# Performance work log

Measured on AMD Instinct MI355X. Metric: run time of the kernel, lower is better.

## Reference

```python
import jax, jax.numpy as jnp
import numpy as np

N, E, M, A, D = 100000, 3200000, 4096, 32, 16
G, V1, V2, O1 = 10, 20, 10, 20


def _lin(key, fin, fout, scale=0.1):
    kw, kb = jax.random.split(key)
    W = jax.random.normal(kw, (fin, fout), jnp.float32) * scale
    b = jax.random.normal(kb, (fout,), jnp.float32) * scale
    return W, b


def setup_inputs():
    key = jax.random.key(0)
    ks = jax.random.split(key, 32)
    inp = {}
    inp["x1"] = jax.random.normal(ks[0], (N, 15), jnp.float32)
    inp["x2"] = jax.random.normal(ks[1], (4,), jnp.float32)
    inp["edges"] = jax.random.randint(ks[2], (2, E), 0, N)
    inp["attack_src"] = jax.random.randint(ks[3], (M, A), 0, N)
    inp["attack_dst"] = jax.random.randint(ks[4], (M, A), 0, N)
    inp["attack_armies"] = jax.random.uniform(ks[5], (M, A), jnp.float32, 1.0, 20.0)
    inp["deploy_target"] = jax.random.randint(ks[6], (M, D), 0, N)
    inp["deploy_armies"] = jax.random.uniform(ks[7], (M, D), jnp.float32, 1.0, 10.0)
    inp["init_W"], inp["init_b"] = _lin(ks[8], 15, G)
    for i, fin in zip((1, 2, 3), (G + 15, 2 * G + 15, 3 * G + 15)):
        k1, k2, k3, k4 = jax.random.split(ks[8 + i], 4)
        inp[f"g{i}_Wl"] = jax.random.normal(k1, (fin, G), jnp.float32) * 0.1
        inp[f"g{i}_Wr"] = jax.random.normal(k2, (fin, G), jnp.float32) * 0.1
        inp[f"g{i}_att"] = jax.random.normal(k3, (G,), jnp.float32) * 0.1
        inp[f"g{i}_b"] = jax.random.normal(k4, (G,), jnp.float32) * 0.1
    inp["vt_W"], inp["vt_b"] = _lin(ks[12], 15 + G + 4, V1)
    inp["va_W"], inp["va_b"] = _lin(ks[13], V1, 1)
    inp["vv_W"], inp["vv_b"] = _lin(ks[14], V1, V2)
    inp["vl_W"], inp["vl_b"] = _lin(ks[15], V2, 1)
    inp["at_W"], inp["at_b"] = _lin(ks[16], 48, O1)
    inp["dt_W"], inp["dt_b"] = _lin(ks[17], 23, O1)
    inp["oa_W"], inp["oa_b"] = _lin(ks[18], O1, 1)
    inp["ov_W"], inp["ov_b"] = _lin(ks[19], O1, 1)
    return inp


def _gatv2(x, src, dst, Wl, Wr, att, bias, n):
    # GATv2 (PyG defaults: heads=1, negative_slope=0.2); dropout omitted (eval mode)
    xl = x @ Wl  # source-side transform  [N, G]
    xr = x @ Wr  # target-side transform  [N, G]
    e = jax.nn.leaky_relu(xl[src] + xr[dst], 0.2) @ att  # [Etot]
    emax = jax.ops.segment_max(e, dst, num_segments=n)
    ex = jnp.exp(e - emax[dst])
    denom = jax.ops.segment_sum(ex, dst, num_segments=n)
    alpha = ex / denom[dst]  # edge softmax per target node
    return jax.ops.segment_sum(alpha[:, None] * xl[src], dst, num_segments=n) + bias


def _forward(x1, x2, edges, attack_src, attack_dst, attack_armies,
             deploy_target, deploy_armies, p):
    n = x1.shape[0]
    loop = jnp.arange(n)
    src = jnp.concatenate([edges[0], loop])  # add_self_loops (PyG default)
    dst = jnp.concatenate([edges[1], loop])
    x_ = jax.nn.relu(x1 @ p["init_W"] + p["init_b"])  # Dropout = identity in eval
    xa = jax.nn.relu(_gatv2(jnp.concatenate([x_, x1], 1), src, dst,
                            p["g1_Wl"], p["g1_Wr"], p["g1_att"], p["g1_b"], n))
    xb = jax.nn.relu(_gatv2(jnp.concatenate([xa, x_, x1], 1), src, dst,
                            p["g2_Wl"], p["g2_Wr"], p["g2_att"], p["g2_b"], n))
    xc = jax.nn.relu(_gatv2(jnp.concatenate([xb, xa, x_, x1], 1), src, dst,
                            p["g3_Wl"], p["g3_Wr"], p["g3_att"], p["g3_b"], n))
    # per-move order features, batched over all moves at once: [M,A,*] / [M,D,*]
    x1d = x1[attack_dst]  # [M, A, 15]
    extra = 0.6 * attack_armies - 0.7 * (x1d[..., 3] + x1d[..., 4])
    att_feat = jnp.concatenate([xc[attack_src], xc[attack_dst],
                                x1[attack_src][..., 3:], x1d[..., 1:],
                                attack_armies[..., None], extra[..., None]], -1)  # [M,A,48]
    dep_feat = jnp.concatenate([xc[deploy_target], x1[deploy_target][..., 3:],
                                deploy_armies[..., None]], -1)  # [M,D,23]
    orders = jax.nn.relu(jnp.concatenate(
        [att_feat @ p["at_W"] + p["at_b"], dep_feat @ p["dt_W"] + p["dt_b"]], 1))  # [M,A+D,O1]
    oattn = jax.nn.softmax(orders @ p["oa_W"] + p["oa_b"], axis=1)  # softmax over orders
    pm = jnp.sum(oattn * (orders @ p["ov_W"] + p["ov_b"]), axis=(1, 2))  # [M]
    # value head: attention-pool over nodes
    vfeat = jnp.concatenate([xc, x1, jnp.tile(x2, (n, 1))], 1)  # [N, 29]
    v = jax.nn.relu(vfeat @ p["vt_W"] + p["vt_b"])
    vattn = jax.nn.softmax(v @ p["va_W"] + p["va_b"], axis=0)
    vagg = jax.nn.relu(jnp.sum(vattn * (v @ p["vv_W"] + p["vv_b"]), axis=0))
    V = jnp.tanh(vagg @ p["vl_W"] + p["vl_b"]).reshape(())
    return V, jax.nn.log_softmax(pm)


def reference(x1, x2, edges, attack_src, attack_dst, attack_armies,
              deploy_target, deploy_armies,
              init_W, init_b,
              g1_Wl, g1_Wr, g1_att, g1_b,
              g2_Wl, g2_Wr, g2_att, g2_b,
              g3_Wl, g3_Wr, g3_att, g3_b,
              vt_W, vt_b, va_W, va_b, vv_W, vv_b, vl_W, vl_b,
              at_W, at_b, dt_W, dt_b, oa_W, oa_b, ov_W, ov_b):
    p = dict(init_W=init_W, init_b=init_b,
             g1_Wl=g1_Wl, g1_Wr=g1_Wr, g1_att=g1_att, g1_b=g1_b,
             g2_Wl=g2_Wl, g2_Wr=g2_Wr, g2_att=g2_att, g2_b=g2_b,
             g3_Wl=g3_Wl, g3_Wr=g3_Wr, g3_att=g3_att, g3_b=g3_b,
             vt_W=vt_W, vt_b=vt_b, va_W=va_W, va_b=va_b, vv_W=vv_W, vv_b=vv_b,
             vl_W=vl_W, vl_b=vl_b, at_W=at_W, at_b=at_b, dt_W=dt_W, dt_b=dt_b,
             oa_W=oa_W, oa_b=oa_b, ov_W=ov_W, ov_b=ov_b)
    return _forward(x1, x2, edges, attack_src, attack_dst, attack_armies,
                    deploy_target, deploy_armies, p)
```

## Files before the change

kernel.cpp:

```cpp
#include <hip/hip_runtime.h>
#include <math.h>


#define PAD 12
#define LP 8
#define MAXB 784
#define CHK 8192

__device__ __forceinline__ float lrelu02(float v) { return v > 0.f ? v : 0.2f * v; }

__device__ __forceinline__ unsigned pk_bf16(float a, float b)
{
    unsigned ua = __float_as_uint(a), ub = __float_as_uint(b);
    ua += 0x7fffu + ((ua >> 16) & 1u);
    ub += 0x7fffu + ((ub >> 16) & 1u);
    return (ua >> 16) | (ub & 0xffff0000u);
}
__device__ __forceinline__ float bf_lo(unsigned u) { return __uint_as_float(u << 16); }
__device__ __forceinline__ float bf_hi(unsigned u) { return __uint_as_float(u & 0xffff0000u); }

template <int NS>
__device__ __forceinline__ void transform_body(
    int n, const float* __restrict__ s0, const float* __restrict__ s1,
    const float* __restrict__ s2, const float* __restrict__ x1,
    const float* __restrict__ Wl, const float* __restrict__ Wr,
    unsigned* __restrict__ XLb, float* __restrict__ XR)
{
    float al[10], ar[10];
#pragma unroll
    for (int g = 0; g < 10; ++g) { al[g] = 0.f; ar[g] = 0.f; }
    int o = 0;
#define TB_BLOCK(SP)                                                        \
    {                                                                       \
        const float4* pr = (const float4*)((SP) + n * PAD);                 \
        float4 v0 = pr[0], v1 = pr[1], v2 = pr[2];                          \
        float fv[10] = {v0.x, v0.y, v0.z, v0.w, v1.x, v1.y, v1.z, v1.w,     \
                        v2.x, v2.y};                                        \
        _Pragma("unroll") for (int k = 0; k < 10; ++k)                      \
        {                                                                   \
            _Pragma("unroll") for (int g = 0; g < 10; ++g)                  \
            {                                                               \
                al[g] += fv[k] * Wl[(o + k) * 10 + g];                      \
                ar[g] += fv[k] * Wr[(o + k) * 10 + g];                      \
            }                                                               \
        }                                                                   \
        o += 10;                                                            \
    }
    if constexpr (NS >= 1) TB_BLOCK(s0)
    if constexpr (NS >= 2) TB_BLOCK(s1)
    if constexpr (NS >= 3) TB_BLOCK(s2)
#undef TB_BLOCK
#pragma unroll
    for (int k = 0; k < 15; ++k) {
        float fv = x1[n * 15 + k];
#pragma unroll
        for (int g = 0; g < 10; ++g) {
            al[g] += fv * Wl[(o + k) * 10 + g];
            ar[g] += fv * Wr[(o + k) * 10 + g];
        }
    }
    uint4 q0;
    q0.x = pk_bf16(al[0], al[1]);
    q0.y = pk_bf16(al[2], al[3]);
    q0.z = pk_bf16(al[4], al[5]);
    q0.w = pk_bf16(al[6], al[7]);
    uint4 q1;
    q1.x = pk_bf16(al[8], al[9]);
    q1.y = 0; q1.z = 0; q1.w = 0;
    uint4* pb = (uint4*)(XLb + (size_t)n * LP);
    pb[0] = q0;
    pb[1] = q1;
    float4* po = (float4*)(XR + n * PAD);
    po[0] = make_float4(ar[0], ar[1], ar[2], ar[3]);
    po[1] = make_float4(ar[4], ar[5], ar[6], ar[7]);
    po[2] = make_float4(ar[8], ar[9], 0.f, 0.f);
}

__global__ __launch_bounds__(256) void k_a1_init(
    const int* __restrict__ edst, int E, unsigned short* __restrict__ pos,
    int* __restrict__ cntg, int PA,
    const float* __restrict__ x1, const float* __restrict__ W,
    const float* __restrict__ b, float* __restrict__ xo, int N, int NBK)
{
    if ((int)blockIdx.x < PA) {
        __shared__ int h[MAXB];
        for (int j = threadIdx.x; j < NBK; j += 256) h[j] = 0;
        __syncthreads();
        int base = blockIdx.x * CHK;
        for (int k = 0; k < CHK / 256; ++k) {
            int i = base + k * 256 + threadIdx.x;
            if (i < E) {
                int bkt = edst[i] >> 7;
                int p = atomicAdd(&h[bkt], 1);
                pos[i] = (unsigned short)p;
            }
        }
        __syncthreads();
        for (int j = threadIdx.x; j < NBK; j += 256)
            cntg[(size_t)j * PA + blockIdx.x] = h[j];
    } else {
        int n = ((int)blockIdx.x - PA) * 256 + (int)threadIdx.x;
        if (n >= N) return;
        float acc[10];
#pragma unroll
        for (int g = 0; g < 10; ++g) acc[g] = b[g];
#pragma unroll
        for (int k = 0; k < 15; ++k) {
            float fv = x1[n * 15 + k];
#pragma unroll
            for (int g = 0; g < 10; ++g) acc[g] += fv * W[k * 10 + g];
        }
        float4* po = (float4*)(xo + n * PAD);
        po[0] = make_float4(fmaxf(acc[0], 0.f), fmaxf(acc[1], 0.f),
                            fmaxf(acc[2], 0.f), fmaxf(acc[3], 0.f));
        po[1] = make_float4(fmaxf(acc[4], 0.f), fmaxf(acc[5], 0.f),
                            fmaxf(acc[6], 0.f), fmaxf(acc[7], 0.f));
        po[2] = make_float4(fmaxf(acc[8], 0.f), fmaxf(acc[9], 0.f), 0.f, 0.f);
    }
}

__global__ __launch_bounds__(1024) void k_scanA(
    const int* __restrict__ cntg, int* __restrict__ bases,
    int* __restrict__ bsumA, int TOT)
{
    __shared__ int wsum[16];
    int t = threadIdx.x;
    int i = blockIdx.x * 1024 + t;
    int lane = t & 63, w = t >> 6;
    int x = (i < TOT) ? cntg[i] : 0;
    int incl = x;
#pragma unroll
    for (int off = 1; off < 64; off <<= 1) {
        int u = __shfl_up(incl, off);
        if (lane >= off) incl += u;
    }
    if (lane == 63) wsum[w] = incl;
    __syncthreads();
    int woff = 0;
    for (int k = 0; k < w; ++k) woff += wsum[k];
    incl += woff;
    if (i < TOT) bases[i] = incl - x;
    if (t == 1023) bsumA[blockIdx.x] = incl;
}

__global__ __launch_bounds__(512) void k_scanB(
    const int* __restrict__ bsumA, int* __restrict__ boffA, int NBLKA,
    float* __restrict__ vsums, int* __restrict__ rowptr, int N, int Etot)
{
    __shared__ int wsum[8];
    int t = threadIdx.x;
    int lane = t & 63, w = t >> 6;
    int x = (t < NBLKA) ? bsumA[t] : 0;
    int incl = x;
#pragma unroll
    for (int off = 1; off < 64; off <<= 1) {
        int u = __shfl_up(incl, off);
        if (lane >= off) incl += u;
    }
    if (lane == 63) wsum[w] = incl;
    __syncthreads();
    int woff = 0;
    for (int k = 0; k < w; ++k) woff += wsum[k];
    incl += woff;
    if (t < NBLKA) boffA[t] = incl - x;
    if (t < 16) vsums[t] = 0.f;
    if (t == 0) rowptr[N] = Etot;
}

__global__ __launch_bounds__(1024) void k_scanC(
    int* __restrict__ bases, const int* __restrict__ boffA, int TOT)
{
    int i = blockIdx.x * 1024 + threadIdx.x;
    if (i < TOT) bases[i] += boffA[blockIdx.x];
}

__global__ __launch_bounds__(256) void k_a2(
    const int* __restrict__ esrc, const int* __restrict__ edst, int E,
    const int* __restrict__ bases, const unsigned short* __restrict__ pos,
    unsigned* __restrict__ pairs, int PA)
{
    int i = blockIdx.x * 256 + threadIdx.x;
    if (i >= E) return;
    int d = edst[i], s = esrc[i];
    int bkt = d >> 7;
    int blk = i / CHK;
    int dest = bases[(size_t)bkt * PA + blk] + (int)pos[i];
    pairs[dest] = (unsigned)s | ((unsigned)(d & 127) << 17);
}

__global__ __launch_bounds__(256) void k_b_tr1(
    const unsigned* __restrict__ pairs, const int* __restrict__ bases,
    int* __restrict__ rowptr, int* __restrict__ deg, int* __restrict__ sidx,
    int N, int NBK, int PA, int E,
    const float* __restrict__ s0a, const float* __restrict__ x1,
    const float* __restrict__ Wl, const float* __restrict__ Wr,
    unsigned* __restrict__ XLb, float* __restrict__ XR, int NB)
{
    if ((int)blockIdx.x < NBK) {
        __shared__ int cnt[128];
        __shared__ int cur[128];
        __shared__ int wtot;
        int t = threadIdx.x;
        if (t < 128) cnt[t] = 0;
        __syncthreads();
        int b = blockIdx.x;
        int p0 = bases[(size_t)b * PA];
        int p1 = (b + 1 < NBK) ? bases[(size_t)(b + 1) * PA] : E;
        int n0 = b << 7;
        int nn = N - n0; nn = nn < 0 ? 0 : (nn > 128 ? 128 : nn);
        for (int i = p0 + t; i < p1; i += 256) atomicAdd(&cnt[pairs[i] >> 17], 1);
        __syncthreads();
        int x = 0, incl = 0;
        if (t < 128) {
            x = cnt[t] + (t < nn ? 1 : 0);
            incl = x;
            int lane = t & 63;
#pragma unroll
            for (int off = 1; off < 64; off <<= 1) {
                int u = __shfl_up(incl, off);
                if (lane >= off) incl += u;
            }
            if (t == 63) wtot = incl;
        }
        __syncthreads();
        int sb = p0 + (b << 7);
        if (t < 128) {
            if (t >= 64) incl += wtot;
            int st = incl - x;
            if (t < nn) {
                int r = sb + st;
                rowptr[n0 + t] = r;
                deg[n0 + t] = cnt[t] + 1;
                sidx[r] = n0 + t;
                cur[t] = st + 1;
            } else {
                cur[t] = st;
            }
        }
        __syncthreads();
        for (int i = p0 + t; i < p1; i += 256) {
            unsigned w = pairs[i];
            int l = w >> 17, s = w & 0x1FFFF;
            int off = atomicAdd(&cur[l], 1);
            sidx[sb + off] = s;
        }
    } else {
        int n = ((int)blockIdx.x - NBK) * 256 + (int)threadIdx.x;
        if (n >= N) return;
        transform_body<1>(n, s0a, nullptr, nullptr, x1, Wl, Wr, XLb, XR);
    }
}

template <int NS>
__global__ __launch_bounds__(256) void k_transform(
    const float* __restrict__ s0, const float* __restrict__ s1,
    const float* __restrict__ s2, const float* __restrict__ x1,
    const float* __restrict__ Wl, const float* __restrict__ Wr,
    unsigned* __restrict__ XLb, float* __restrict__ XR, int N)
{
    int n = blockIdx.x * blockDim.x + threadIdx.x;
    if (n >= N) return;
    transform_body<NS>(n, s0, s1, s2, x1, Wl, Wr, XLb, XR);
}

__global__ __launch_bounds__(256) void k_gather(
    const int* __restrict__ rowptr, const int* __restrict__ deg,
    const int* __restrict__ sidx,
    const unsigned* __restrict__ XLb, const float* __restrict__ XR,
    const float* __restrict__ att, const float* __restrict__ b,
    float* __restrict__ xo, int N)
{
    int node = blockIdx.x * 16 + (threadIdx.x >> 4);
    int l16 = threadIdx.x & 15;
    float acc[10];
#pragma unroll
    for (int g = 0; g < 10; ++g) acc[g] = 0.f;
    float den = 0.f;
    float satt[10];
#pragma unroll
    for (int g = 0; g < 10; ++g) satt[g] = att[g];
    if (node < N) {
        const float4* pr = (const float4*)(XR + node * PAD);
        float4 r0 = pr[0], r1 = pr[1], r2 = pr[2];
        float xr[10] = {r0.x, r0.y, r0.z, r0.w, r1.x, r1.y, r1.z, r1.w, r2.x, r2.y};
        int start = rowptr[node];
        int dgr = deg[node];
        int j = l16;
        while (j + 16 < dgr) {
            int s0 = sidx[start + j];
            int s1 = sidx[start + j + 16];
            const unsigned* pl0 = XLb + (size_t)s0 * LP;
            const unsigned* pl1 = XLb + (size_t)s1 * LP;
            uint4 qa = *(const uint4*)pl0;
            unsigned qa4 = pl0[4];
            uint4 qb = *(const uint4*)pl1;
            unsigned qb4 = pl1[4];
            float xa[10] = {bf_lo(qa.x), bf_hi(qa.x), bf_lo(qa.y), bf_hi(qa.y),
                            bf_lo(qa.z), bf_hi(qa.z), bf_lo(qa.w), bf_hi(qa.w),
                            bf_lo(qa4), bf_hi(qa4)};
            float xb[10] = {bf_lo(qb.x), bf_hi(qb.x), bf_lo(qb.y), bf_hi(qb.y),
                            bf_lo(qb.z), bf_hi(qb.z), bf_lo(qb.w), bf_hi(qb.w),
                            bf_lo(qb4), bf_hi(qb4)};
            float ea = 0.f, eb = 0.f;
#pragma unroll
            for (int g = 0; g < 10; ++g) {
                ea += lrelu02(xa[g] + xr[g]) * satt[g];
                eb += lrelu02(xb[g] + xr[g]) * satt[g];
            }
            float exa = __expf(ea), exb = __expf(eb);
#pragma unroll
            for (int g = 0; g < 10; ++g) acc[g] += exa * xa[g] + exb * xb[g];
            den += exa + exb;
            j += 32;
        }
        if (j < dgr) {
            int s = sidx[start + j];
            const unsigned* pl = XLb + (size_t)s * LP;
            uint4 q = *(const uint4*)pl;
            unsigned q4 = pl[4];
            float xl[10] = {bf_lo(q.x), bf_hi(q.x), bf_lo(q.y), bf_hi(q.y),
                            bf_lo(q.z), bf_hi(q.z), bf_lo(q.w), bf_hi(q.w),
                            bf_lo(q4), bf_hi(q4)};
            float e = 0.f;
#pragma unroll
            for (int g = 0; g < 10; ++g) e += lrelu02(xl[g] + xr[g]) * satt[g];
            float ex = __expf(e);
#pragma unroll
            for (int g = 0; g < 10; ++g) acc[g] += ex * xl[g];
            den += ex;
        }
    }
#pragma unroll
    for (int off = 1; off < 16; off <<= 1) {
        den += __shfl_xor(den, off);
#pragma unroll
        for (int g = 0; g < 10; ++g) acc[g] += __shfl_xor(acc[g], off);
    }
    if (node < N && l16 == 0) {
        float inv = 1.f / den;
        float r[10];
#pragma unroll
        for (int g = 0; g < 10; ++g) r[g] = fmaxf(acc[g] * inv + b[g], 0.f);
        float4* po = (float4*)(xo + node * PAD);
        po[0] = make_float4(r[0], r[1], r[2], r[3]);
        po[1] = make_float4(r[4], r[5], r[6], r[7]);
        po[2] = make_float4(r[8], r[9], 0.f, 0.f);
    }
}

__global__ __launch_bounds__(256) void k_value_policy(
    const float* __restrict__ xc, const float* __restrict__ x1,
    const float* __restrict__ x2,
    const float* __restrict__ vtW, const float* __restrict__ vtb,
    const float* __restrict__ vaW, const float* __restrict__ vab,
    const float* __restrict__ vvW, const float* __restrict__ vvb,
    float* __restrict__ vsums,
    const int* __restrict__ asrc, const int* __restrict__ adst,
    const float* __restrict__ aarm,
    const int* __restrict__ dtgt, const float* __restrict__ darm,
    const float* __restrict__ atW, const float* __restrict__ atb,
    const float* __restrict__ dtW, const float* __restrict__ dtb,
    const float* __restrict__ oaW, const float* __restrict__ oab,
    const float* __restrict__ ovW, const float* __restrict__ ovb,
    float* __restrict__ pm, int NB, int N, int M)
{
    if ((int)blockIdx.x < NB) {
        __shared__ float sred[4][11];
        int t = threadIdx.x;
        int n = blockIdx.x * blockDim.x + t;
        float w = 0.f;
        float wv[10];
#pragma unroll
        for (int c = 0; c < 10; ++c) wv[c] = 0.f;
        if (n < N) {
            float v[20];
#pragma unroll
            for (int j = 0; j < 20; ++j) v[j] = vtb[j];
            {
                const float4* pc = (const float4*)(xc + n * PAD);
                float4 c0 = pc[0], c1 = pc[1], c2 = pc[2];
                float fv[10] = {c0.x, c0.y, c0.z, c0.w, c1.x, c1.y, c1.z, c1.w,
                                c2.x, c2.y};
#pragma unroll
                for (int k = 0; k < 10; ++k)
#pragma unroll
                    for (int j = 0; j < 20; ++j) v[j] += fv[k] * vtW[k * 20 + j];
            }
#pragma unroll
            for (int k = 0; k < 15; ++k) {
                float fv = x1[n * 15 + k];
#pragma unroll
                for (int j = 0; j < 20; ++j) v[j] += fv * vtW[(10 + k) * 20 + j];
            }
#pragma unroll
            for (int k = 0; k < 4; ++k) {
                float fv = x2[k];
#pragma unroll
                for (int j = 0; j < 20; ++j) v[j] += fv * vtW[(25 + k) * 20 + j];
            }
            float sc = vab[0];
#pragma unroll
            for (int j = 0; j < 20; ++j) {
                v[j] = fmaxf(v[j], 0.f);
                sc += v[j] * vaW[j];
            }
            w = __expf(sc);
#pragma unroll
            for (int c = 0; c < 10; ++c) {
                float t2 = vvb[c];
#pragma unroll
                for (int j = 0; j < 20; ++j) t2 += v[j] * vvW[j * 10 + c];
                wv[c] = w * t2;
            }
        }
#pragma unroll
        for (int off = 32; off > 0; off >>= 1) {
            w += __shfl_xor(w, off);
#pragma unroll
            for (int c = 0; c < 10; ++c) wv[c] += __shfl_xor(wv[c], off);
        }
        int wave = t >> 6, lane = t & 63;
        if (lane == 0) {
            sred[wave][0] = w;
#pragma unroll
            for (int c = 0; c < 10; ++c) sred[wave][1 + c] = wv[c];
        }
        __syncthreads();
        if (t == 0) {
#pragma unroll
            for (int c = 0; c < 11; ++c) {
                float s = sred[0][c] + sred[1][c] + sred[2][c] + sred[3][c];
                atomicAdd(&vsums[c], s);
            }
        }
    } else {
        int wave = threadIdx.x >> 6, lane = threadIdx.x & 63;
        int m = ((int)blockIdx.x - NB) * 4 + wave;
        float asc = -1e30f, vsc = 0.f;
        if (m < M) {
            float ord[20];
            bool have = false;
            if (lane < 32) {
                int a = lane;
                int s = asrc[m * 32 + a], d = adst[m * 32 + a];
                float arm = aarm[m * 32 + a];
#pragma unroll
                for (int j = 0; j < 20; ++j) ord[j] = atb[j];
                {
                    const float4* pc = (const float4*)(xc + s * PAD);
                    float4 c0 = pc[0], c1 = pc[1], c2 = pc[2];
                    float fv[10] = {c0.x, c0.y, c0.z, c0.w, c1.x, c1.y, c1.z,
                                    c1.w, c2.x, c2.y};
#pragma unroll
                    for (int k = 0; k < 10; ++k)
#pragma unroll
                        for (int j = 0; j < 20; ++j)
                            ord[j] += fv[k] * atW[k * 20 + j];
                }
                {
                    const float4* pc = (const float4*)(xc + d * PAD);
                    float4 c0 = pc[0], c1 = pc[1], c2 = pc[2];
                    float fv[10] = {c0.x, c0.y, c0.z, c0.w, c1.x, c1.y, c1.z,
                                    c1.w, c2.x, c2.y};
#pragma unroll
                    for (int k = 0; k < 10; ++k)
#pragma unroll
                        for (int j = 0; j < 20; ++j)
                            ord[j] += fv[k] * atW[(10 + k) * 20 + j];
                }
#pragma unroll
                for (int k = 0; k < 12; ++k) {
                    float fv = x1[s * 15 + 3 + k];
#pragma unroll
                    for (int j = 0; j < 20; ++j)
                        ord[j] += fv * atW[(20 + k) * 20 + j];
                }
                float d3 = 0.f, d4 = 0.f;
#pragma unroll
                for (int k = 0; k < 14; ++k) {
                    float fv = x1[d * 15 + 1 + k];
                    if (k == 2) d3 = fv;
                    if (k == 3) d4 = fv;
#pragma unroll
                    for (int j = 0; j < 20; ++j)
                        ord[j] += fv * atW[(32 + k) * 20 + j];
                }
                float extra = 0.6f * arm - 0.7f * (d3 + d4);
#pragma unroll
                for (int j = 0; j < 20; ++j)
                    ord[j] += arm * atW[46 * 20 + j] + extra * atW[47 * 20 + j];
                have = true;
            } else if (lane < 48) {
                int dd = lane - 32;
                int tg = dtgt[m * 16 + dd];
                float arm = darm[m * 16 + dd];
#pragma unroll
                for (int j = 0; j < 20; ++j) ord[j] = dtb[j];
                {
                    const float4* pc = (const float4*)(xc + tg * PAD);
                    float4 c0 = pc[0], c1 = pc[1], c2 = pc[2];
                    float fv[10] = {c0.x, c0.y, c0.z, c0.w, c1.x, c1.y, c1.z,
                                    c1.w, c2.x, c2.y};
#pragma unroll
                    for (int k = 0; k < 10; ++k)
#pragma unroll
                        for (int j = 0; j < 20; ++j)
                            ord[j] += fv[k] * dtW[k * 20 + j];
                }
#pragma unroll
                for (int k = 0; k < 12; ++k) {
                    float fv = x1[tg * 15 + 3 + k];
#pragma unroll
                    for (int j = 0; j < 20; ++j)
                        ord[j] += fv * dtW[(10 + k) * 20 + j];
                }
#pragma unroll
                for (int j = 0; j < 20; ++j) ord[j] += arm * dtW[22 * 20 + j];
                have = true;
            }
            if (have) {
                asc = oab[0]; vsc = ovb[0];
#pragma unroll
                for (int j = 0; j < 20; ++j) {
                    float oj = fmaxf(ord[j], 0.f);
                    asc += oj * oaW[j];
                    vsc += oj * ovW[j];
                }
            }
        }
        float mx = asc;
#pragma unroll
        for (int off = 32; off > 0; off >>= 1) mx = fmaxf(mx, __shfl_xor(mx, off));
        float p = (asc > -1e29f) ? __expf(asc - mx) : 0.f;
        float num = p * vsc;
        float Z = p;
#pragma unroll
        for (int off = 32; off > 0; off >>= 1) {
            Z += __shfl_xor(Z, off);
            num += __shfl_xor(num, off);
        }
        if (m < M && lane == 0) pm[m] = num / Z;
    }
}

__global__ __launch_bounds__(1024) void k_final(
    const float* __restrict__ pm, const float* __restrict__ vsums,
    const float* __restrict__ vlW, const float* __restrict__ vlb,
    float* __restrict__ out, int M)
{
    __shared__ float red[16];
    __shared__ float sval;
    int t = threadIdx.x;
    int wave = t >> 6, lane = t & 63;
    if (t == 1023) {
        float inv = 1.f / vsums[0];
        float V = vlb[0];
#pragma unroll
        for (int j = 0; j < 10; ++j) V += fmaxf(vsums[1 + j] * inv, 0.f) * vlW[j];
        out[0] = tanhf(V);
    }
    float mx = -1e30f;
    for (int i = t; i < M; i += 1024) mx = fmaxf(mx, pm[i]);
#pragma unroll
    for (int off = 32; off > 0; off >>= 1) mx = fmaxf(mx, __shfl_xor(mx, off));
    if (lane == 0) red[wave] = mx;
    __syncthreads();
    if (t == 0) {
        float m2 = red[0];
        for (int i = 1; i < 16; ++i) m2 = fmaxf(m2, red[i]);
        sval = m2;
    }
    __syncthreads();
    float smax = sval;
    float sum = 0.f;
    for (int i = t; i < M; i += 1024) sum += __expf(pm[i] - smax);
#pragma unroll
    for (int off = 32; off > 0; off >>= 1) sum += __shfl_xor(sum, off);
    if (lane == 0) red[wave] = sum;
    __syncthreads();
    if (t == 0) {
        float s2 = 0.f;
        for (int i = 0; i < 16; ++i) s2 += red[i];
        sval = s2;
    }
    __syncthreads();
    float lse = smax + logf(sval);
    for (int i = t; i < M; i += 1024) out[1 + i] = pm[i] - lse;
}

extern "C" void kernel_launch(void* const* d_in, const int* in_sizes, int n_in,
                              void* d_out, int out_size, void* d_ws, size_t ws_size,
                              hipStream_t stream)
{
    const float* x1   = (const float*)d_in[0];
    const float* x2   = (const float*)d_in[1];
    const int*   edges = (const int*)d_in[2];
    const int*   asrc = (const int*)d_in[3];
    const int*   adst = (const int*)d_in[4];
    const float* aarm = (const float*)d_in[5];
    const int*   dtgt = (const int*)d_in[6];
    const float* darm = (const float*)d_in[7];
    const float* initW = (const float*)d_in[8];
    const float* initb = (const float*)d_in[9];
    const float* g1Wl = (const float*)d_in[10];
    const float* g1Wr = (const float*)d_in[11];
    const float* g1att = (const float*)d_in[12];
    const float* g1b = (const float*)d_in[13];
    const float* g2Wl = (const float*)d_in[14];
    const float* g2Wr = (const float*)d_in[15];
    const float* g2att = (const float*)d_in[16];
    const float* g2b = (const float*)d_in[17];
    const float* g3Wl = (const float*)d_in[18];
    const float* g3Wr = (const float*)d_in[19];
    const float* g3att = (const float*)d_in[20];
    const float* g3b = (const float*)d_in[21];
    const float* vtW = (const float*)d_in[22];
    const float* vtb = (const float*)d_in[23];
    const float* vaW = (const float*)d_in[24];
    const float* vab = (const float*)d_in[25];
    const float* vvW = (const float*)d_in[26];
    const float* vvb = (const float*)d_in[27];
    const float* vlW = (const float*)d_in[28];
    const float* vlb = (const float*)d_in[29];
    const float* atW = (const float*)d_in[30];
    const float* atb = (const float*)d_in[31];
    const float* dtW = (const float*)d_in[32];
    const float* dtb = (const float*)d_in[33];
    const float* oaW = (const float*)d_in[34];
    const float* oab = (const float*)d_in[35];
    const float* ovW = (const float*)d_in[36];
    const float* ovb = (const float*)d_in[37];

    const int N = in_sizes[0] / 15;
    const int E = in_sizes[2] / 2;
    const int M = in_sizes[3] / 32;
    const int Etot = E + N;
    const int NBK = (N + 127) >> 7;
    const int PA = (E + CHK - 1) / CHK;
    const int TOT = NBK * PA;

    float* ws = (float*)d_ws;
    size_t off = 0;
    float* XU = ws + off; off += (size_t)N * PAD;
    float* XA = ws + off; off += (size_t)N * PAD;
    float* XB = ws + off; off += (size_t)N * PAD;
    float* XC = ws + off; off += (size_t)N * PAD;
    unsigned* XLb = (unsigned*)(ws + off); off += (size_t)N * LP;
    float* XR = ws + off; off += (size_t)N * PAD;
    int* sidx = (int*)(ws + off); off += Etot;
    unsigned* pairs = (unsigned*)(ws + off); off += E;
    int* deg = (int*)(ws + off); off += N;
    int* rowptr = (int*)(ws + off); off += N + 8;
    int* cntg = (int*)(ws + off); off += TOT + 8;
    int* bases = (int*)(ws + off); off += TOT + 8;
    int* bsumA = (int*)(ws + off); off += 512;
    int* boffA = (int*)(ws + off); off += 512;
    float* VS = ws + off; off += 16;
    float* PM = ws + off; off += M;
    unsigned short* pos = (unsigned short*)XA;

    float* outp = (float*)d_out;

    const int NB = (N + 255) / 256;
    const int NG = (N + 15) / 16;
    const int PB = (M + 3) / 4;
    const int SCA = (TOT + 1023) / 1024;
    const int* esrc = edges;
    const int* edst = edges + E;

    k_a1_init<<<PA + NB, 256, 0, stream>>>(edst, E, pos, cntg, PA,
                                           x1, initW, initb, XU, N, NBK);
    k_scanA<<<SCA, 1024, 0, stream>>>(cntg, bases, bsumA, TOT);
    k_scanB<<<1, 512, 0, stream>>>(bsumA, boffA, SCA, VS, rowptr, N, Etot);
    k_scanC<<<SCA, 1024, 0, stream>>>(bases, boffA, TOT);
    k_a2<<<(E + 255) / 256, 256, 0, stream>>>(esrc, edst, E, bases, pos, pairs, PA);
    k_b_tr1<<<NBK + NB, 256, 0, stream>>>(pairs, bases, rowptr, deg, sidx, N, NBK, PA, E,
                                          XU, x1, g1Wl, g1Wr, XLb, XR, NB);
    k_gather<<<NG, 256, 0, stream>>>(rowptr, deg, sidx, XLb, XR, g1att, g1b, XA, N);

    k_transform<2><<<NB, 256, 0, stream>>>(XA, XU, nullptr, x1, g2Wl, g2Wr, XLb, XR, N);
    k_gather<<<NG, 256, 0, stream>>>(rowptr, deg, sidx, XLb, XR, g2att, g2b, XB, N);

    k_transform<3><<<NB, 256, 0, stream>>>(XB, XA, XU, x1, g3Wl, g3Wr, XLb, XR, N);
    k_gather<<<NG, 256, 0, stream>>>(rowptr, deg, sidx, XLb, XR, g3att, g3b, XC, N);

    k_value_policy<<<NB + PB, 256, 0, stream>>>(XC, x1, x2, vtW, vtb, vaW, vab,
                                                vvW, vvb, VS, asrc, adst, aarm,
                                                dtgt, darm, atW, atb, dtW, dtb,
                                                oaW, oab, ovW, ovb, PM, NB, N, M);
    k_final<<<1, 1024, 0, stream>>>(PM, VS, vlW, vlb, outp, M);
}
```

Before: 395.0 us.

## Split policy scoring into dense per-option threads and a separate softmax kernel

Attack and deploy option scoring move out of the combined value/policy kernel. Previously one wave handled one move, leaving 16 of 64 lanes idle and keeping attack and deploy paths divergent within the wave. Now each thread scores a single attack or deploy option in its own block range and writes (score, value) pairs to a workspace buffer. A new small kernel then does the per-move softmax-weighted reduction. This adds an extra launch and a global write/read of M*48 float2 values in exchange for removing the idle lanes and the divergence.

```diff
diff --git a/kernel.cpp b/kernel.cpp
--- a/kernel.cpp
+++ b/kernel.cpp
@@ -348,13 +348,9 @@
     }
 }
 
-__global__ __launch_bounds__(256) void k_value_policy(
+__global__ __launch_bounds__(256) void k_scores(
     const float* __restrict__ xc, const float* __restrict__ x1,
     const float* __restrict__ x2,
-    const float* __restrict__ vtW, const float* __restrict__ vtb,
-    const float* __restrict__ vaW, const float* __restrict__ vab,
-    const float* __restrict__ vvW, const float* __restrict__ vvb,
-    float* __restrict__ vsums,
     const int* __restrict__ asrc, const int* __restrict__ adst,
     const float* __restrict__ aarm,
     const int* __restrict__ dtgt, const float* __restrict__ darm,
@@ -362,12 +358,108 @@
     const float* __restrict__ dtW, const float* __restrict__ dtb,
     const float* __restrict__ oaW, const float* __restrict__ oab,
     const float* __restrict__ ovW, const float* __restrict__ ovb,
-    float* __restrict__ pm, int NB, int N, int M)
-{
-    if ((int)blockIdx.x < NB) {
+    const float* __restrict__ vtW, const float* __restrict__ vtb,
+    const float* __restrict__ vaW, const float* __restrict__ vab,
+    const float* __restrict__ vvW, const float* __restrict__ vvb,
+    float* __restrict__ vsums, float2* __restrict__ OS,
+    int AB, int DB, int NB, int N, int M)
+{
+    if ((int)blockIdx.x < AB) {
+        int i = blockIdx.x * 256 + threadIdx.x;
+        if (i >= M * 32) return;
+        int m = i >> 5, a = i & 31;
+        int s = asrc[i], d = adst[i];
+        float arm = aarm[i];
+        float ord[20];
+#pragma unroll
+        for (int j = 0; j < 20; ++j) ord[j] = atb[j];
+        {
+            const float4* pc = (const float4*)(xc + s * PAD);
+            float4 c0 = pc[0], c1 = pc[1], c2 = pc[2];
+            float fv[10] = {c0.x, c0.y, c0.z, c0.w, c1.x, c1.y, c1.z, c1.w,
+                            c2.x, c2.y};
+#pragma unroll
+            for (int k = 0; k < 10; ++k)
+#pragma unroll
+                for (int j = 0; j < 20; ++j) ord[j] += fv[k] * atW[k * 20 + j];
+        }
+        {
+            const float4* pc = (const float4*)(xc + d * PAD);
+            float4 c0 = pc[0], c1 = pc[1], c2 = pc[2];
+            float fv[10] = {c0.x, c0.y, c0.z, c0.w, c1.x, c1.y, c1.z, c1.w,
+                            c2.x, c2.y};
+#pragma unroll
+            for (int k = 0; k < 10; ++k)
+#pragma unroll
+                for (int j = 0; j < 20; ++j)
+                    ord[j] += fv[k] * atW[(10 + k) * 20 + j];
+        }
+#pragma unroll
+        for (int k = 0; k < 12; ++k) {
+            float fv = x1[s * 15 + 3 + k];
+#pragma unroll
+            for (int j = 0; j < 20; ++j) ord[j] += fv * atW[(20 + k) * 20 + j];
+        }
+        float d3 = 0.f, d4 = 0.f;
+#pragma unroll
+        for (int k = 0; k < 14; ++k) {
+            float fv = x1[d * 15 + 1 + k];
+            if (k == 2) d3 = fv;
+            if (k == 3) d4 = fv;
+#pragma unroll
+            for (int j = 0; j < 20; ++j) ord[j] += fv * atW[(32 + k) * 20 + j];
+        }
+        float extra = 0.6f * arm - 0.7f * (d3 + d4);
+#pragma unroll
+        for (int j = 0; j < 20; ++j)
+            ord[j] += arm * atW[46 * 20 + j] + extra * atW[47 * 20 + j];
+        float asc = oab[0], vsc = ovb[0];
+#pragma unroll
+        for (int j = 0; j < 20; ++j) {
+            float oj = fmaxf(ord[j], 0.f);
+            asc += oj * oaW[j];
+            vsc += oj * ovW[j];
+        }
+        OS[(size_t)m * 48 + a] = make_float2(asc, vsc);
+    } else if ((int)blockIdx.x < AB + DB) {
+        int i = ((int)blockIdx.x - AB) * 256 + threadIdx.x;
+        if (i >= M * 16) return;
+        int m = i >> 4, dd = i & 15;
+        int tg = dtgt[i];
+        float arm = darm[i];
+        float ord[20];
+#pragma unroll
+        for (int j = 0; j < 20; ++j) ord[j] = dtb[j];
+        {
+            const float4* pc = (const float4*)(xc + tg * PAD);
+            float4 c0 = pc[0], c1 = pc[1], c2 = pc[2];
+            float fv[10] = {c0.x, c0.y, c0.z, c0.w, c1.x, c1.y, c1.z, c1.w,
+                            c2.x, c2.y};
+#pragma unroll
+            for (int k = 0; k < 10; ++k)
+#pragma unroll
+                for (int j = 0; j < 20; ++j) ord[j] += fv[k] * dtW[k * 20 + j];
+        }
+#pragma unroll
+        for (int k = 0; k < 12; ++k) {
+            float fv = x1[tg * 15 + 3 + k];
+#pragma unroll
+            for (int j = 0; j < 20; ++j) ord[j] += fv * dtW[(10 + k) * 20 + j];
+        }
+#pragma unroll
+        for (int j = 0; j < 20; ++j) ord[j] += arm * dtW[22 * 20 + j];
+        float asc = oab[0], vsc = ovb[0];
+#pragma unroll
+        for (int j = 0; j < 20; ++j) {
+            float oj = fmaxf(ord[j], 0.f);
+            asc += oj * oaW[j];
+            vsc += oj * ovW[j];
+        }
+        OS[(size_t)m * 48 + 32 + dd] = make_float2(asc, vsc);
+    } else {
         __shared__ float sred[4][11];
         int t = threadIdx.x;
-        int n = blockIdx.x * blockDim.x + t;
+        int n = ((int)blockIdx.x - AB - DB) * 256 + t;
         float w = 0.f;
         float wv[10];
 #pragma unroll
@@ -433,114 +525,26 @@
                 atomicAdd(&vsums[c], s);
             }
         }
-    } else {
-        int wave = threadIdx.x >> 6, lane = threadIdx.x & 63;
-        int m = ((int)blockIdx.x - NB) * 4 + wave;
-        float asc = -1e30f, vsc = 0.f;
-        if (m < M) {
-            float ord[20];
-            bool have = false;
-            if (lane < 32) {
-                int a = lane;
-                int s = asrc[m * 32 + a], d = adst[m * 32 + a];
-                float arm = aarm[m * 32 + a];
-#pragma unroll
-                for (int j = 0; j < 20; ++j) ord[j] = atb[j];
-                {
-                    const float4* pc = (const float4*)(xc + s * PAD);
-                    float4 c0 = pc[0], c1 = pc[1], c2 = pc[2];
-                    float fv[10] = {c0.x, c0.y, c0.z, c0.w, c1.x, c1.y, c1.z,
-                                    c1.w, c2.x, c2.y};
-#pragma unroll
-                    for (int k = 0; k < 10; ++k)
-#pragma unroll
-                        for (int j = 0; j < 20; ++j)
-                            ord[j] += fv[k] * atW[k * 20 + j];
-                }
-                {
-                    const float4* pc = (const float4*)(xc + d * PAD);
-                    float4 c0 = pc[0], c1 = pc[1], c2 = pc[2];
-                    float fv[10] = {c0.x, c0.y, c0.z, c0.w, c1.x, c1.y, c1.z,
-                                    c1.w, c2.x, c2.y};
-#pragma unroll
-                    for (int k = 0; k < 10; ++k)
-#pragma unroll
-                        for (int j = 0; j < 20; ++j)
-                            ord[j] += fv[k] * atW[(10 + k) * 20 + j];
-                }
-#pragma unroll
-                for (int k = 0; k < 12; ++k) {
-                    float fv = x1[s * 15 + 3 + k];
-#pragma unroll
-                    for (int j = 0; j < 20; ++j)
-                        ord[j] += fv * atW[(20 + k) * 20 + j];
-                }
-                float d3 = 0.f, d4 = 0.f;
-#pragma unroll
-                for (int k = 0; k < 14; ++k) {
-                    float fv = x1[d * 15 + 1 + k];
-                    if (k == 2) d3 = fv;
-                    if (k == 3) d4 = fv;
-#pragma unroll
-                    for (int j = 0; j < 20; ++j)
-                        ord[j] += fv * atW[(32 + k) * 20 + j];
-                }
-                float extra = 0.6f * arm - 0.7f * (d3 + d4);
-#pragma unroll
-                for (int j = 0; j < 20; ++j)
-                    ord[j] += arm * atW[46 * 20 + j] + extra * atW[47 * 20 + j];
-                have = true;
-            } else if (lane < 48) {
-                int dd = lane - 32;
-                int tg = dtgt[m * 16 + dd];
-                float arm = darm[m * 16 + dd];
-#pragma unroll
-                for (int j = 0; j < 20; ++j) ord[j] = dtb[j];
-                {
-                    const float4* pc = (const float4*)(xc + tg * PAD);
-                    float4 c0 = pc[0], c1 = pc[1], c2 = pc[2];
-                    float fv[10] = {c0.x, c0.y, c0.z, c0.w, c1.x, c1.y, c1.z,
-                                    c1.w, c2.x, c2.y};
-#pragma unroll
-                    for (int k = 0; k < 10; ++k)
-#pragma unroll
-                        for (int j = 0; j < 20; ++j)
-                            ord[j] += fv[k] * dtW[k * 20 + j];
-                }
-#pragma unroll
-                for (int k = 0; k < 12; ++k) {
-                    float fv = x1[tg * 15 + 3 + k];
-#pragma unroll
-                    for (int j = 0; j < 20; ++j)
-                        ord[j] += fv * dtW[(10 + k) * 20 + j];
-                }
-#pragma unroll
-                for (int j = 0; j < 20; ++j) ord[j] += arm * dtW[22 * 20 + j];
-                have = true;
-            }
-            if (have) {
-                asc = oab[0]; vsc = ovb[0];
-#pragma unroll
-                for (int j = 0; j < 20; ++j) {
-                    float oj = fmaxf(ord[j], 0.f);
-                    asc += oj * oaW[j];
-                    vsc += oj * ovW[j];
-                }
-            }
-        }
-        float mx = asc;
-#pragma unroll
-        for (int off = 32; off > 0; off >>= 1) mx = fmaxf(mx, __shfl_xor(mx, off));
-        float p = (asc > -1e29f) ? __expf(asc - mx) : 0.f;
-        float num = p * vsc;
-        float Z = p;
-#pragma unroll
-        for (int off = 32; off > 0; off >>= 1) {
-            Z += __shfl_xor(Z, off);
-            num += __shfl_xor(num, off);
-        }
-        if (m < M && lane == 0) pm[m] = num / Z;
-    }
+    }
+}
+
+__global__ __launch_bounds__(256) void k_moves(
+    const float2* __restrict__ OS, float* __restrict__ pm, int M)
+{
+    int m = blockIdx.x * 256 + threadIdx.x;
+    if (m >= M) return;
+    const float2* p = OS + (size_t)m * 48;
+    float mx = -1e30f;
+#pragma unroll
+    for (int o = 0; o < 48; ++o) mx = fmaxf(mx, p[o].x);
+    float Z = 0.f, num = 0.f;
+#pragma unroll
+    for (int o = 0; o < 48; ++o) {
+        float e = __expf(p[o].x - mx);
+        Z += e;
+        num += e * p[o].y;
+    }
+    pm[m] = num / Z;
 }
 
 __global__ __launch_bounds__(1024) void k_final(
@@ -657,13 +661,15 @@
     int* boffA = (int*)(ws + off); off += 512;
     float* VS = ws + off; off += 16;
     float* PM = ws + off; off += M;
+    float2* OS = (float2*)(ws + off); off += (size_t)M * 48 * 2;
     unsigned short* pos = (unsigned short*)XA;
 
     float* outp = (float*)d_out;
 
     const int NB = (N + 255) / 256;
     const int NG = (N + 15) / 16;
-    const int PB = (M + 3) / 4;
+    const int AB = (M * 32 + 255) / 256;
+    const int DB = (M * 16 + 255) / 256;
     const int SCA = (TOT + 1023) / 1024;
     const int* esrc = edges;
     const int* edst = edges + E;
@@ -684,9 +690,11 @@
     k_transform<3><<<NB, 256, 0, stream>>>(XB, XA, XU, x1, g3Wl, g3Wr, XLb, XR, N);
     k_gather<<<NG, 256, 0, stream>>>(rowptr, deg, sidx, XLb, XR, g3att, g3b, XC, N);
 
-    k_value_policy<<<NB + PB, 256, 0, stream>>>(XC, x1, x2, vtW, vtb, vaW, vab,
-                                                vvW, vvb, VS, asrc, adst, aarm,
-                                                dtgt, darm, atW, atb, dtW, dtb,
-                                                oaW, oab, ovW, ovb, PM, NB, N, M);
+    k_scores<<<AB + DB + NB, 256, 0, stream>>>(XC, x1, x2, asrc, adst, aarm,
+                                               dtgt, darm, atW, atb, dtW, dtb,
+                                               oaW, oab, ovW, ovb,
+                                               vtW, vtb, vaW, vab, vvW, vvb,
+                                               VS, OS, AB, DB, NB, N, M);
+    k_moves<<<(M + 255) / 256, 256, 0, stream>>>(OS, PM, M);
     k_final<<<1, 1024, 0, stream>>>(PM, VS, vlW, vlb, outp, M);
 }
```

After: 405.2 us. +2.6%, slower.
